# Kernel tuning notes

Hardware: AMD Instinct MI355X
Metric: run time of the kernel (lower is better)

Reference implementation:

```python
import jax, jax.numpy as jnp
import numpy as np

B, H_IMG, W_IMG, K = 4, 60, 80, 8
HW = H_IMG * W_IMG
IMG_D, PT_D = 192, 128
NH, DH = 6, 64
INNER = NH * DH
NHF = 6
POS_D = 2 * (2 * NHF + 1)  # harmonic emb of 2-d offset, append_input=True -> 26
MAX_DIST = 0.1


def setup_inputs() -> dict:
    key = jax.random.key(0)
    ks = jax.random.split(key, 6)
    ys, xs = jnp.meshgrid(jnp.linspace(0.0, 1.0, H_IMG), jnp.linspace(0.0, 1.0, W_IMG), indexing='ij')
    img_uv = jnp.stack([xs.reshape(-1), ys.reshape(-1)], axis=-1)  # [HW, 2], normalized pixel grid
    return {
        'feat_2d': jax.random.normal(ks[0], (B, HW, IMG_D), jnp.float32),
        'feat_3d': jax.random.normal(ks[1], (B, HW, PT_D), jnp.float32),
        'proj_uv': jax.random.uniform(ks[2], (B, HW, 2), dtype=jnp.float32),
        'img_uv': img_uv,
        'ln_gamma': jnp.ones((IMG_D,), jnp.float32),
        'q_gamma': jnp.ones((NH, DH), jnp.float32),
        'k_gamma': jnp.ones((NH, DH), jnp.float32),
        'Wq': jax.random.normal(ks[3], (IMG_D, INNER), jnp.float32) * IMG_D ** -0.5,
        'Wkv': jax.random.normal(ks[4], (PT_D + POS_D, 2 * INNER), jnp.float32) * (PT_D + POS_D) ** -0.5,
        'Wout': jax.random.normal(ks[5], (INNER, INNER), jnp.float32) * INNER ** -0.5,
    }


def _layernorm(x, g, eps=1e-5):
    mu = jnp.mean(x, -1, keepdims=True)
    var = jnp.mean((x - mu) ** 2, -1, keepdims=True)
    return (x - mu) * jax.lax.rsqrt(var + eps) * g


def _rmsnorm(x, g):
    # lucidrains-style query/key RMSNorm: l2-normalize last dim, scale by sqrt(dim) * per-head gamma
    n = jnp.maximum(jnp.linalg.norm(x, axis=-1, keepdims=True), 1e-12)
    return x / n * (DH ** 0.5) * g


def reference(feat_2d, feat_3d, proj_uv, img_uv, ln_gamma, q_gamma, k_gamma, Wq, Wkv, Wout):
    # --- kNN: for each image pixel, k nearest projected points (brute force) ---
    d2 = (jnp.sum(img_uv ** 2, -1)[None, :, None]
          + jnp.sum(proj_uv ** 2, -1)[:, None, :]
          - 2.0 * jnp.einsum('qd,bnd->bqn', img_uv, proj_uv))  # [B, HW, HW]
    idx = jax.lax.top_k(-d2, K)[1]  # [B, HW, K] int32 indices

    # --- gather neighbor uv coords and 3d features ---
    knn_uv = img_uv[idx]                                        # [B, HW, K, 2]
    knn_f3 = jnp.take_along_axis(feat_3d, idx.reshape(B, HW * K, 1), axis=1).reshape(B, HW, K, PT_D)
    offset = knn_uv - img_uv[None, :, None, :]                  # [B, HW, K, 2]
    mask = jnp.sum(offset ** 2, -1) <= MAX_DIST ** 2            # [B, HW, K]

    # --- harmonic positional embedding of offsets ---
    freqs = 2.0 ** jnp.arange(NHF, dtype=jnp.float32)
    e = (offset[..., None] * freqs).reshape(B, HW, K, 2 * NHF)
    pos = jnp.concatenate([jnp.sin(e), jnp.cos(e), offset], -1)  # [B, HW, K, 26]

    # --- Q / K / V projections ---
    q = (_layernorm(feat_2d, ln_gamma) @ Wq).reshape(B, HW, NH, DH)
    kv = jnp.concatenate([knn_f3, pos], -1) @ Wkv               # [B, HW, K, 2*INNER]
    k_, v_ = jnp.split(kv, 2, axis=-1)
    k_ = k_.reshape(B, HW, K, NH, DH)
    v_ = v_.reshape(B, HW, K, NH, DH)
    q = _rmsnorm(q, q_gamma)
    k_ = _rmsnorm(k_, k_gamma)

    # --- tiny per-pixel attention (query len 1, key len K), scale=1.0 ---
    scores = jnp.einsum('bnhd,bnkhd->bnhk', q, k_)              # [B, HW, NH, K]
    scores = jnp.where(mask[:, :, None, :], scores, -1e30)
    attn = jax.nn.softmax(scores, axis=-1)
    out = jnp.einsum('bnhk,bnkhd->bnhd', attn, v_).reshape(B, HW, INNER)
    return out @ Wout  # output_type='1d': [B, HW, INNER]
```

## Files before the change

### kernel.cpp

```cpp
#include <hip/hip_runtime.h>
#include <math.h>

#define B_    4
#define HW_   4800
#define K_    8
#define IMGD  192
#define PTD   128
#define NH_   6
#define DH_   64
#define INNER 384
#define KVIN  154
#define QT    8
#define NJ    64
#define XBS   168
#define AST   392
#define KTQ   6
#define KTK   5
#define KTO   12

#define GC    64
#define NCELL (GC * GC)
#define CS    (1.0f / 64.0f)

typedef _Float16 f16;
typedef __attribute__((ext_vector_type(8))) _Float16 f16x8;
typedef __attribute__((ext_vector_type(4))) float f32x4;

__global__ __launch_bounds__(256) void pack_kernel(
    const float* __restrict__ Wq, const float* __restrict__ Wkv,
    const float* __restrict__ Wout, f16* __restrict__ pw)
{
  const int e = blockIdx.x * 256 + threadIdx.x;
  if (e >= 672 * 512) return;
  const int f = e >> 9, r = e & 511, l = r >> 3, j = r & 7;
  const int lm = l & 15, kin = (l >> 4) * 8 + j;
  float v;
  if (f < 144) {
    const int nt = f / 6, kt = f % 6;
    v = Wq[(size_t)(kt * 32 + kin) * INNER + nt * 16 + lm];
  } else if (f < 264) {
    const int g = f - 144, nt = g / 5, kt = g % 5, k = kt * 32 + kin;
    v = (k < KVIN) ? Wkv[(size_t)k * (2 * INNER) + nt * 16 + lm] : 0.f;
  } else if (f < 384) {
    const int g = f - 264, nt = g / 5, kt = g % 5, k = kt * 32 + kin;
    v = (k < KVIN) ? Wkv[(size_t)k * (2 * INNER) + INNER + nt * 16 + lm] : 0.f;
  } else {
    const int g = f - 384, nt = g / 12, kt = g % 12;
    v = Wout[(size_t)(kt * 32 + kin) * INNER + nt * 16 + lm];
  }
  pw[e] = (f16)v;
}

__global__ __launch_bounds__(1024) void build_kernel(
    const float* __restrict__ proj_uv,
    float2* __restrict__ spts,
    unsigned short* __restrict__ sidx,
    unsigned short* __restrict__ cstart)
{
  __shared__ unsigned cnt[NCELL];
  __shared__ unsigned start[NCELL];
  __shared__ unsigned wsum[16];

  const int b   = blockIdx.x;
  const int tid = threadIdx.x;
  const int lane = tid & 63, wid = tid >> 6;
  const float2* pv = reinterpret_cast<const float2*>(proj_uv + (size_t)b * HW_ * 2);

  for (int c = tid; c < NCELL; c += 1024) cnt[c] = 0u;
  __syncthreads();

  for (int i = tid; i < HW_; i += 1024) {
    const float2 p = pv[i];
    const int cx = min(GC - 1, max(0, (int)(p.x * GC)));
    const int cy = min(GC - 1, max(0, (int)(p.y * GC)));
    atomicAdd(&cnt[cy * GC + cx], 1u);
  }
  __syncthreads();

  const int c0 = tid * 4;
  const unsigned v0 = cnt[c0], v1 = cnt[c0 + 1], v2 = cnt[c0 + 2], v3 = cnt[c0 + 3];
  const unsigned mysum = v0 + v1 + v2 + v3;
  unsigned inc = mysum;
#pragma unroll
  for (int off = 1; off < 64; off <<= 1) {
    const unsigned u = (unsigned)__shfl_up((int)inc, off);
    if (lane >= off) inc += u;
  }
  if (lane == 63) wsum[wid] = inc;
  __syncthreads();
  if (tid == 0) {
    unsigned s = 0;
#pragma unroll
    for (int wv = 0; wv < 16; ++wv) { const unsigned t = wsum[wv]; wsum[wv] = s; s += t; }
  }
  __syncthreads();
  unsigned base = wsum[wid] + inc - mysum;
  start[c0] = base;
  start[c0 + 1] = base + v0;
  start[c0 + 2] = base + v0 + v1;
  start[c0 + 3] = base + v0 + v1 + v2;
  unsigned short* cs = cstart + (size_t)b * (NCELL + 1);
  cs[c0]     = (unsigned short)start[c0];
  cs[c0 + 1] = (unsigned short)start[c0 + 1];
  cs[c0 + 2] = (unsigned short)start[c0 + 2];
  cs[c0 + 3] = (unsigned short)start[c0 + 3];
  if (tid == 0) cs[NCELL] = (unsigned short)HW_;
  __syncthreads();

  for (int i = tid; i < HW_; i += 1024) {
    const float2 p = pv[i];
    const int cx = min(GC - 1, max(0, (int)(p.x * GC)));
    const int cy = min(GC - 1, max(0, (int)(p.y * GC)));
    const unsigned slot = atomicAdd(&start[cy * GC + cx], 1u);
    spts[(size_t)b * HW_ + slot] = p;
    sidx[(size_t)b * HW_ + slot] = (unsigned short)i;
  }
}

#define SCAN_CELL(cyv, cxv)                                                   \
  {                                                                           \
    const int c = (cyv) * GC + (cxv);                                         \
    const int s0 = s_cs[c], s1 = s_cs[c + 1];                                 \
    for (int s = s0; s < s1; ++s) {                                           \
      const float2 p = s_p[s];                                                \
      const int n = (int)s_i[s];                                              \
      const float sqp = p.x * p.x + p.y * p.y;                \
      const float dot = fmaf(qy, p.y, qx * p.x);            \
      const float d   = (sqq + sqp) - 2.0f * dot;                             \
      const bool enter = (d < dist[K_ - 1]) ||                                \
                         (d == dist[K_ - 1] && n < ind[K_ - 1]);              \
      if (enter) {                                                            \
        bool placed = false;                                                  \
        _Pragma("unroll")                                                     \
        for (int t = K_ - 1; t >= 1; --t) {                                   \
          if (!placed) {                                                      \
            const bool lt = (d < dist[t - 1]) ||                              \
                            (d == dist[t - 1] && n < ind[t - 1]);             \
            if (lt) { dist[t] = dist[t - 1]; ind[t] = ind[t - 1]; }           \
            else    { dist[t] = d; ind[t] = n; placed = true; }               \
          }                                                                   \
        }                                                                     \
        if (!placed) { dist[0] = d; ind[0] = n; }                             \
      }                                                                       \
    }                                                                         \
  }

__global__ __launch_bounds__(256) void knn_kernel(
    const float* __restrict__ img_uv,
    const float2* __restrict__ spts,
    const unsigned short* __restrict__ sidx,
    const unsigned short* __restrict__ cstart,
    int* __restrict__ idx_out)
{
#pragma clang fp contract(off)
  __shared__ float2 s_p[HW_];
  __shared__ unsigned short s_i[HW_];
  __shared__ unsigned short s_cs[NCELL + 1];

  const int tid = threadIdx.x;
  const int b   = blockIdx.y;
  const int q   = blockIdx.x * 256 + tid;

  {
    const float2* gp = spts + (size_t)b * HW_;
    const unsigned short* gi = sidx + (size_t)b * HW_;
    const unsigned short* gc = cstart + (size_t)b * (NCELL + 1);
    for (int i = tid; i < HW_; i += 256) { s_p[i] = gp[i]; s_i[i] = gi[i]; }
    for (int i = tid; i < NCELL + 1; i += 256) s_cs[i] = gc[i];
  }
  __syncthreads();
  if (q >= HW_) return;

  const float qx = img_uv[q * 2 + 0];
  const float qy = img_uv[q * 2 + 1];
  const float sqq = qx * qx + qy * qy;

  const int cellx = min(GC - 1, max(0, (int)(qx * GC)));
  const int celly = min(GC - 1, max(0, (int)(qy * GC)));

  float dist[K_];
  int   ind[K_];
#pragma unroll
  for (int s = 0; s < K_; ++s) { dist[s] = 3.4e38f; ind[s] = 0x7fffffff; }

  for (int r = 0; r < GC; ++r) {
    if (r >= 2 && dist[K_ - 1] < 1e38f) {
      const float rb = (float)(r - 1) * CS;
      if (rb * rb > dist[K_ - 1] + 1e-4f) break;
    }
    const int ylo = max(0, celly - r), yhi = min(GC - 1, celly + r);
    for (int cy = ylo; cy <= yhi; ++cy) {
      const bool edge = (cy == celly - r) || (cy == celly + r);
      if (edge) {
        const int xlo = max(0, cellx - r), xhi = min(GC - 1, cellx + r);
        for (int cx = xlo; cx <= xhi; ++cx) SCAN_CELL(cy, cx);
      } else {
        if (cellx - r >= 0)      SCAN_CELL(cy, cellx - r);
        if (cellx + r <= GC - 1) SCAN_CELL(cy, cellx + r);
      }
    }
  }

  int* dst = idx_out + ((size_t)b * HW_ + q) * K_;
#pragma unroll
  for (int s = 0; s < K_; ++s) dst[s] = ind[s];
}

__global__ __launch_bounds__(256, 3) void fused_kernel(
    const float* __restrict__ feat_2d,
    const float* __restrict__ feat_3d,
    const float* __restrict__ img_uv,
    const float* __restrict__ ln_gamma,
    const float* __restrict__ q_gamma,
    const float* __restrict__ k_gamma,
    const f16*   __restrict__ pw,
    const int*   __restrict__ idx_ws,
    float* __restrict__ out)
{
  __shared__ alignas(16) f16   s_X[NJ][XBS];
  __shared__ alignas(16) float s_regA[QT * AST];
  __shared__ alignas(16) float s_attn[QT][NH_][K_];
  __shared__ alignas(16) float s_kss[NJ][NH_];
  __shared__ alignas(16) float s_ksc[NJ][NH_];
  __shared__ float s_qss[QT][NH_];
  __shared__ float s_mask[NJ];
  __shared__ int   s_idx[NJ];
  __shared__ float s_offx[NJ];
  __shared__ float s_offy[NJ];

  f16* s_f16 = reinterpret_cast<f16*>(s_regA);

  const int tid = threadIdx.x;
  const int b   = blockIdx.y;
  const int bx  = (blockIdx.x & 7) * 75 + (blockIdx.x >> 3);
  const int q0  = bx * QT;
  const int l   = tid & 63;
  const int w   = tid >> 6;
  const int lm  = l & 15;
  const int lg  = l >> 4;

  const f16* pwq = pw;
  const f16* pwk = pw + 144 * 512;
  const f16* pwv = pw + 264 * 512;
  const f16* pwo = pw + 384 * 512;

  if (tid < NJ) {
    const int j  = tid;
    const int q  = q0 + (j >> 3);
    const int id = idx_ws[((size_t)b * HW_ + q) * K_ + (j & 7)];
    s_idx[j] = id;
    const float ax = img_uv[id * 2], ay = img_uv[id * 2 + 1];
    const float bx2 = img_uv[q * 2], by2 = img_uv[q * 2 + 1];
    s_offx[j] = ax - bx2; s_offy[j] = ay - by2;
    const double dox = (double)ax - (double)bx2;
    const double doy = (double)ay - (double)by2;
    s_mask[j] = (dox * dox + doy * doy <= 0.010000000000000002) ? 1.f : 0.f;
  }
  {
    unsigned* z = (unsigned*)(s_f16 + 8 * AST);
    for (int o = tid; o < 4 * AST; o += 256) z[o] = 0u;
  }
  if (tid < QT * NH_) s_qss[tid / NH_][tid % NH_] = 0.f;
  for (int o = tid; o < NJ * NH_; o += 256) {
    s_kss[o / NH_][o % NH_] = 0.f;
    s_ksc[o / NH_][o % NH_] = 0.f;
  }
  {
    const int r  = ((tid >> 6) << 1) | ((tid >> 5) & 1);
    const int sl = tid & 31;
    const float* row = feat_2d + ((size_t)b * HW_ + q0 + r) * IMGD;
    float x[6]; float sum = 0.f, ssq = 0.f;
#pragma unroll
    for (int i = 0; i < 6; ++i) { x[i] = row[sl + 32 * i]; sum += x[i]; ssq += x[i] * x[i]; }
#pragma unroll
    for (int m = 16; m >= 1; m >>= 1) { sum += __shfl_xor(sum, m); ssq += __shfl_xor(ssq, m); }
    const float mu = sum * (1.f / 192.f);
    float var = ssq * (1.f / 192.f) - mu * mu;
    var = fmaxf(var, 0.f);
    const float rstd = rsqrtf(var + 1e-5f);
#pragma unroll
    for (int i = 0; i < 6; ++i) {
      const int c = sl + 32 * i;
      s_f16[r * AST + c] = (f16)((x[i] - mu) * rstd * ln_gamma[c]);
    }
  }
  __syncthreads();

  const int jX = tid >> 2, tsub = tid & 3;
  float4 xf[8];
  {
    const float4* f4 = reinterpret_cast<const float4*>(
        feat_3d + ((size_t)b * HW_ + s_idx[jX]) * PTD) + tsub * 8;
#pragma unroll
    for (int i = 0; i < 8; ++i) xf[i] = f4[i];
  }
  f32x4 qacc[6];
#pragma unroll
  for (int t = 0; t < 6; ++t) qacc[t] = (f32x4){0.f, 0.f, 0.f, 0.f};
  {
    const f16* ar = s_f16 + lm * AST + lg * 8;
    f16x8 acur = *(const f16x8*)(ar);
    f16x8 bcur[6], bnxt[6];
#pragma unroll
    for (int t = 0; t < 6; ++t)
      bcur[t] = *(const f16x8*)(pwq + ((((w * 6 + t) * 6 + 0) << 6) + l) * 8);
#pragma unroll
    for (int kt = 0; kt < KTQ; ++kt) {
      f16x8 anxt;
      if (kt < KTQ - 1) {
        anxt = *(const f16x8*)(ar + (kt + 1) * 32);
#pragma unroll
        for (int t = 0; t < 6; ++t)
          bnxt[t] = *(const f16x8*)(pwq + ((((w * 6 + t) * 6 + kt + 1) << 6) + l) * 8);
      }
#pragma unroll
      for (int t = 0; t < 6; ++t)
        qacc[t] = __builtin_amdgcn_mfma_f32_16x16x32_f16(acur, bcur[t], qacc[t], 0, 0, 0);
      if (kt < KTQ - 1) {
        acur = anxt;
#pragma unroll
        for (int t = 0; t < 6; ++t) bcur[t] = bnxt[t];
      }
    }
  }
  {
    f16* xr = &s_X[jX][tsub * 32];
#pragma unroll
    for (int i = 0; i < 8; ++i) {
      xr[i * 4 + 0] = (f16)xf[i].x; xr[i * 4 + 1] = (f16)xf[i].y;
      xr[i * 4 + 2] = (f16)xf[i].z; xr[i * 4 + 3] = (f16)xf[i].w;
    }
    if (tsub == 0) {
      const float ox = s_offx[jX], oy = s_offy[jX];
      f16* xp = &s_X[jX][PTD];
#pragma unroll
      for (int m = 0; m < 6; ++m) {
        const float fr = (float)(1 << m);
        float sx, cx, sy, cy;
        sincosf(ox * fr, &sx, &cx);
        sincosf(oy * fr, &sy, &cy);
        xp[m] = (f16)sx; xp[6 + m] = (f16)sy;
        xp[12 + m] = (f16)cx; xp[18 + m] = (f16)cy;
      }
      xp[24] = (f16)ox; xp[25] = (f16)oy;
#pragma unroll
      for (int m = 26; m < 32; ++m) xp[m] = (f16)0.f;
    }
  }
  __syncthreads();

  if (lg < 2) {
    const int h0w = (w * 6) >> 2;
    float s2a[4], s2b[4];
#pragma unroll
    for (int reg = 0; reg < 4; ++reg) { s2a[reg] = 0.f; s2b[reg] = 0.f; }
#pragma unroll
    for (int t = 0; t < 6; ++t) {
      const int hi = ((w * 6 + t) >> 2) - h0w;
#pragma unroll
      for (int reg = 0; reg < 4; ++reg) {
        const float v = qacc[t][reg];
        s_regA[(lg * 4 + reg) * AST + (w * 6 + t) * 16 + lm] = v;
        if (hi == 0) s2a[reg] += v * v; else s2b[reg] += v * v;
      }
    }
#pragma unroll
    for (int reg = 0; reg < 4; ++reg) {
      atomicAdd(&s_qss[lg * 4 + reg][h0w], s2a[reg]);
      atomicAdd(&s_qss[lg * 4 + reg][h0w + 1], s2b[reg]);
    }
  }
  __syncthreads();

  {
    f16x8 af[4][KTK];
#pragma unroll
    for (int mt = 0; mt < 4; ++mt) {
      const f16* xh = &s_X[16 * mt + lm][lg * 8];
#pragma unroll
      for (int kt = 0; kt < KTK; ++kt) af[mt][kt] = *(const f16x8*)(xh + kt * 32);
    }
    f16x8 bcur[KTK], bnxt[KTK];
#pragma unroll
    for (int kt = 0; kt < KTK; ++kt)
      bcur[kt] = *(const f16x8*)(pwk + (((w * KTK + kt) << 6) + l) * 8);
#pragma unroll
    for (int h = 0; h < NH_; ++h) {
      if (h < NH_ - 1) {
        const int ntn = (h + 1) * 4 + w;
#pragma unroll
        for (int kt = 0; kt < KTK; ++kt)
          bnxt[kt] = *(const f16x8*)(pwk + (((ntn * KTK + kt) << 6) + l) * 8);
      }
      const int nt  = h * 4 + w;
      const int col = nt * 16 + lm;
      const float gg = k_gamma[col] * q_gamma[col];
      f32x4 c[4];
#pragma unroll
      for (int mt = 0; mt < 4; ++mt) c[mt] = (f32x4){0.f, 0.f, 0.f, 0.f};
#pragma unroll
      for (int kt = 0; kt < KTK; ++kt)
#pragma unroll
        for (int mt = 0; mt < 4; ++mt)
          c[mt] = __builtin_amdgcn_mfma_f32_16x16x32_f16(af[mt][kt], bcur[kt], c[mt], 0, 0, 0);
#pragma unroll
      for (int mt = 0; mt < 4; ++mt) {
        const int rq = 2 * mt + (lg >> 1);
        const float nnq = fmaxf(sqrtf(s_qss[rq][h]), 1e-12f);
        const float qg = s_regA[rq * AST + col] * (8.f / nnq) * gg;
        float ss[4], sc[4];
#pragma unroll
        for (int reg = 0; reg < 4; ++reg) {
          const float v = c[mt][reg];
          ss[reg] = v * v; sc[reg] = v * qg;
        }
#pragma unroll
        for (int m = 1; m < 16; m <<= 1) {
#pragma unroll
          for (int reg = 0; reg < 4; ++reg) {
            ss[reg] += __shfl_xor(ss[reg], m);
            sc[reg] += __shfl_xor(sc[reg], m);
          }
        }
        if (lm == 0) {
#pragma unroll
          for (int reg = 0; reg < 4; ++reg) {
            const int row = 16 * mt + 4 * lg + reg;
            atomicAdd(&s_kss[row][h], ss[reg]);
            atomicAdd(&s_ksc[row][h], sc[reg]);
          }
        }
      }
      if (h < NH_ - 1) {
#pragma unroll
        for (int kt = 0; kt < KTK; ++kt) bcur[kt] = bnxt[kt];
      }
    }
  }
  __syncthreads();

  if (tid < QT * NH_) {
    const int r = tid / NH_, h = tid % NH_;
    float s[K_]; float mx = -1e38f;
#pragma unroll
    for (int k = 0; k < K_; ++k) {
      const int row = r * K_ + k;
      const float nn = fmaxf(sqrtf(s_kss[row][h]), 1e-12f);
      float v = (8.f / nn) * s_ksc[row][h];
      if (s_mask[row] == 0.f) v = -1e30f;
      s[k] = v; mx = fmaxf(mx, v);
    }
    float sum = 0.f;
#pragma unroll
    for (int k = 0; k < K_; ++k) { const float pp = expf(s[k] - mx); s[k] = pp; sum += pp; }
    const float inv = 1.f / sum;
#pragma unroll
    for (int k = 0; k < K_; ++k) s_attn[r][h][k] = s[k] * inv;
  }
  __syncthreads();

  {
    unsigned* z = (unsigned*)(s_f16 + 8 * AST);
    for (int o = tid; o < 4 * AST; o += 256) z[o] = 0u;
  }
  f16x8 xbv[4];
#pragma unroll
  for (int rep = 0; rep < 4; ++rep) {
    const int task = tid + 256 * rep;
    if (task < 960) {
      const int p = task / 320, rem = task - p * 320;
      const int r16 = rem / 20, cb = rem - r16 * 20;
      const int q = r16 & 7, hh = 2 * p + (r16 >> 3);
      const float4 a0 = *(const float4*)&s_attn[q][hh][0];
      const float4 a1 = *(const float4*)&s_attn[q][hh][4];
      const float av[8] = {a0.x, a0.y, a0.z, a0.w, a1.x, a1.y, a1.z, a1.w};
      float acc[8];
#pragma unroll
      for (int e = 0; e < 8; ++e) acc[e] = 0.f;
#pragma unroll
      for (int k = 0; k < 8; ++k) {
        const f16x8 xv = *(const f16x8*)&s_X[q * 8 + k][cb * 8];
#pragma unroll
        for (int e = 0; e < 8; ++e) acc[e] += av[k] * (float)xv[e];
      }
      f16x8 rr;
#pragma unroll
      for (int e = 0; e < 8; ++e) rr[e] = (f16)acc[e];
      xbv[rep] = rr;
    }
  }
  __syncthreads();
#pragma unroll
  for (int rep = 0; rep < 4; ++rep) {
    const int task = tid + 256 * rep;
    if (task < 960) {
      const int p = task / 320, rem = task - p * 320;
      const int r16 = rem / 20, cb = rem - r16 * 20;
      *(f16x8*)&s_X[p * 16 + r16][cb * 8] = xbv[rep];
    }
  }
  __syncthreads();

  {
#pragma unroll
    for (int p = 0; p < 3; ++p) {
      f16x8 af[KTK];
#pragma unroll
      for (int kt = 0; kt < KTK; ++kt)
        af[kt] = *(const f16x8*)&s_X[p * 16 + lm][lg * 8 + kt * 32];
#pragma unroll
      for (int ii = 0; ii < 2; ++ii) {
        const int nt = w + 4 * (2 * p + ii);
        const int h  = nt >> 2;
        f32x4 c = (f32x4){0.f, 0.f, 0.f, 0.f};
#pragma unroll
        for (int kt = 0; kt < KTK; ++kt) {
          const f16x8 bf = *(const f16x8*)(pwv + (((nt * KTK + kt) << 6) + l) * 8);
          c = __builtin_amdgcn_mfma_f32_16x16x32_f16(af[kt], bf, c, 0, 0, 0);
        }
        if ((lg >> 1) == (h & 1)) {
#pragma unroll
          for (int reg = 0; reg < 4; ++reg) {
            const int q = (lg * 4 + reg) & 7;
            s_f16[q * AST + nt * 16 + lm] = (f16)c[reg];
          }
        }
      }
    }
  }
  __syncthreads();

  {
    f32x4 oacc[6];
#pragma unroll
    for (int t = 0; t < 6; ++t) oacc[t] = (f32x4){0.f, 0.f, 0.f, 0.f};
    const f16* ar = s_f16 + lm * AST + lg * 8;
    f16x8 acur = *(const f16x8*)(ar);
    f16x8 bcur[6], bnxt[6];
#pragma unroll
    for (int t = 0; t < 6; ++t)
      bcur[t] = *(const f16x8*)(pwo + ((((w * 6 + t) * 12 + 0) << 6) + l) * 8);
#pragma unroll
    for (int kt = 0; kt < KTO; ++kt) {
      f16x8 anxt;
      if (kt < KTO - 1) {
        anxt = *(const f16x8*)(ar + (kt + 1) * 32);
#pragma unroll
        for (int t = 0; t < 6; ++t)
          bnxt[t] = *(const f16x8*)(pwo + ((((w * 6 + t) * 12 + kt + 1) << 6) + l) * 8);
      }
#pragma unroll
      for (int t = 0; t < 6; ++t)
        oacc[t] = __builtin_amdgcn_mfma_f32_16x16x32_f16(acur, bcur[t], oacc[t], 0, 0, 0);
      if (kt < KTO - 1) {
        acur = anxt;
#pragma unroll
        for (int t = 0; t < 6; ++t) bcur[t] = bnxt[t];
      }
    }
    if (lg < 2) {
      float* orow0 = out + ((size_t)b * HW_ + q0) * INNER;
#pragma unroll
      for (int reg = 0; reg < 4; ++reg) {
        const int m = lg * 4 + reg;
#pragma unroll
        for (int t = 0; t < 6; ++t) {
          orow0[(size_t)m * INNER + (w * 6 + t) * 16 + lm] = oacc[t][reg];
        }
      }
    }
  }
}

extern "C" void kernel_launch(void* const* d_in, const int* in_sizes, int n_in,
                              void* d_out, int out_size, void* d_ws, size_t ws_size,
                              hipStream_t stream) {
  (void)in_sizes; (void)n_in; (void)out_size; (void)ws_size;
  const float* feat_2d = (const float*)d_in[0];
  const float* feat_3d = (const float*)d_in[1];
  const float* proj_uv = (const float*)d_in[2];
  const float* img_uv  = (const float*)d_in[3];
  const float* ln_g    = (const float*)d_in[4];
  const float* q_g     = (const float*)d_in[5];
  const float* k_g     = (const float*)d_in[6];
  const float* Wq      = (const float*)d_in[7];
  const float* Wkv     = (const float*)d_in[8];
  const float* Wout    = (const float*)d_in[9];
  float* out = (float*)d_out;

  int* idx_ws = (int*)d_ws;
  f16* pw = (f16*)((char*)d_ws + 614400);
  float2* spts = (float2*)((char*)d_ws + 1302528);
  unsigned short* sidx = (unsigned short*)((char*)d_ws + 1456128);
  unsigned short* cstart = (unsigned short*)((char*)d_ws + 1494528);

  pack_kernel<<<dim3(1344), 256, 0, stream>>>(Wq, Wkv, Wout, pw);
  build_kernel<<<dim3(B_), 1024, 0, stream>>>(proj_uv, spts, sidx, cstart);
  knn_kernel<<<dim3((HW_ + 255) / 256, B_), 256, 0, stream>>>(
      img_uv, spts, sidx, cstart, idx_ws);
  fused_kernel<<<dim3(HW_ / QT, B_), 256, 0, stream>>>(
      feat_2d, feat_3d, img_uv, ln_g, q_g, k_g, pw, idx_ws, out);
}
```

Baseline: 261.9 us.

## Double query tile to 16 pixels per block to fill MFMA rows

Raises the per-block query tile from 8 to 16 pixels (128 neighbor rows), so the 16-row MFMA tiles for Q, output and V projections are fully used instead of half-padded with zeros. The zero-fill of padding rows goes away, K-projection weights are held in registers across 8 row tiles, and the V step is restructured per head. The trade is roughly doubled shared memory and register use per block, so occupancy drops from 3 to 2 blocks per CU, and the block-to-XCD remap is reworked for 300 blocks.

After: 292.3 us. +11.6%, slower.

```diff
diff --git a/kernel.cpp b/kernel.cpp
--- a/kernel.cpp
+++ b/kernel.cpp
@@ -10,8 +10,8 @@
 #define DH_   64
 #define INNER 384
 #define KVIN  154
-#define QT    8
-#define NJ    64
+#define QT    16
+#define NJ    128
 #define XBS   168
 #define AST   392
 #define KTQ   6
@@ -206,7 +206,7 @@
   for (int s = 0; s < K_; ++s) dst[s] = ind[s];
 }
 
-__global__ __launch_bounds__(256, 3) void fused_kernel(
+__global__ __launch_bounds__(256, 2) void fused_kernel(
     const float* __restrict__ feat_2d,
     const float* __restrict__ feat_3d,
     const float* __restrict__ img_uv,
@@ -232,7 +232,9 @@
 
   const int tid = threadIdx.x;
   const int b   = blockIdx.y;
-  const int bx  = (blockIdx.x & 7) * 75 + (blockIdx.x >> 3);
+  const int orig = blockIdx.x;
+  const int xcd  = orig & 7, id8 = orig >> 3;
+  const int bx   = (xcd < 4) ? xcd * 38 + id8 : 152 + (xcd - 4) * 37 + id8;
   const int q0  = bx * QT;
   const int l   = tid & 63;
   const int w   = tid >> 6;
@@ -256,79 +258,48 @@
     const double doy = (double)ay - (double)by2;
     s_mask[j] = (dox * dox + doy * doy <= 0.010000000000000002) ? 1.f : 0.f;
   }
-  {
-    unsigned* z = (unsigned*)(s_f16 + 8 * AST);
-    for (int o = tid; o < 4 * AST; o += 256) z[o] = 0u;
-  }
   if (tid < QT * NH_) s_qss[tid / NH_][tid % NH_] = 0.f;
   for (int o = tid; o < NJ * NH_; o += 256) {
     s_kss[o / NH_][o % NH_] = 0.f;
     s_ksc[o / NH_][o % NH_] = 0.f;
   }
   {
-    const int r  = ((tid >> 6) << 1) | ((tid >> 5) & 1);
-    const int sl = tid & 31;
+    const int r  = tid >> 4;
+    const int sl = tid & 15;
     const float* row = feat_2d + ((size_t)b * HW_ + q0 + r) * IMGD;
-    float x[6]; float sum = 0.f, ssq = 0.f;
-#pragma unroll
-    for (int i = 0; i < 6; ++i) { x[i] = row[sl + 32 * i]; sum += x[i]; ssq += x[i] * x[i]; }
-#pragma unroll
-    for (int m = 16; m >= 1; m >>= 1) { sum += __shfl_xor(sum, m); ssq += __shfl_xor(ssq, m); }
+    float x[12]; float sum = 0.f, ssq = 0.f;
+#pragma unroll
+    for (int i = 0; i < 12; ++i) { x[i] = row[sl + 16 * i]; sum += x[i]; ssq += x[i] * x[i]; }
+#pragma unroll
+    for (int m = 8; m >= 1; m >>= 1) { sum += __shfl_xor(sum, m); ssq += __shfl_xor(ssq, m); }
     const float mu = sum * (1.f / 192.f);
     float var = ssq * (1.f / 192.f) - mu * mu;
     var = fmaxf(var, 0.f);
     const float rstd = rsqrtf(var + 1e-5f);
 #pragma unroll
-    for (int i = 0; i < 6; ++i) {
-      const int c = sl + 32 * i;
+    for (int i = 0; i < 12; ++i) {
+      const int c = sl + 16 * i;
       s_f16[r * AST + c] = (f16)((x[i] - mu) * rstd * ln_gamma[c]);
     }
   }
   __syncthreads();
 
-  const int jX = tid >> 2, tsub = tid & 3;
-  float4 xf[8];
+  const int jX = tid >> 1, tsub = tid & 1;
   {
     const float4* f4 = reinterpret_cast<const float4*>(
-        feat_3d + ((size_t)b * HW_ + s_idx[jX]) * PTD) + tsub * 8;
-#pragma unroll
-    for (int i = 0; i < 8; ++i) xf[i] = f4[i];
-  }
-  f32x4 qacc[6];
-#pragma unroll
-  for (int t = 0; t < 6; ++t) qacc[t] = (f32x4){0.f, 0.f, 0.f, 0.f};
-  {
-    const f16* ar = s_f16 + lm * AST + lg * 8;
-    f16x8 acur = *(const f16x8*)(ar);
-    f16x8 bcur[6], bnxt[6];
-#pragma unroll
-    for (int t = 0; t < 6; ++t)
-      bcur[t] = *(const f16x8*)(pwq + ((((w * 6 + t) * 6 + 0) << 6) + l) * 8);
-#pragma unroll
-    for (int kt = 0; kt < KTQ; ++kt) {
-      f16x8 anxt;
-      if (kt < KTQ - 1) {
-        anxt = *(const f16x8*)(ar + (kt + 1) * 32);
-#pragma unroll
-        for (int t = 0; t < 6; ++t)
-          bnxt[t] = *(const f16x8*)(pwq + ((((w * 6 + t) * 6 + kt + 1) << 6) + l) * 8);
-      }
-#pragma unroll
-      for (int t = 0; t < 6; ++t)
-        qacc[t] = __builtin_amdgcn_mfma_f32_16x16x32_f16(acur, bcur[t], qacc[t], 0, 0, 0);
-      if (kt < KTQ - 1) {
-        acur = anxt;
-#pragma unroll
-        for (int t = 0; t < 6; ++t) bcur[t] = bnxt[t];
-      }
-    }
-  }
-  {
-    f16* xr = &s_X[jX][tsub * 32];
-#pragma unroll
-    for (int i = 0; i < 8; ++i) {
-      xr[i * 4 + 0] = (f16)xf[i].x; xr[i * 4 + 1] = (f16)xf[i].y;
-      xr[i * 4 + 2] = (f16)xf[i].z; xr[i * 4 + 3] = (f16)xf[i].w;
+        feat_3d + ((size_t)b * HW_ + s_idx[jX]) * PTD) + tsub * 16;
+    f16* xr = &s_X[jX][tsub * 64];
+#pragma unroll
+    for (int half = 0; half < 2; ++half) {
+      float4 xf[8];
+#pragma unroll
+      for (int i = 0; i < 8; ++i) xf[i] = f4[half * 8 + i];
+#pragma unroll
+      for (int i = 0; i < 8; ++i) {
+        const int c = half * 32 + i * 4;
+        xr[c + 0] = (f16)xf[i].x; xr[c + 1] = (f16)xf[i].y;
+        xr[c + 2] = (f16)xf[i].z; xr[c + 3] = (f16)xf[i].w;
+      }
     }
     if (tsub == 0) {
       const float ox = s_offx[jX], oy = s_offy[jX];
@@ -347,9 +318,38 @@
       for (int m = 26; m < 32; ++m) xp[m] = (f16)0.f;
     }
   }
-  __syncthreads();
-
-  if (lg < 2) {
+  f32x4 qacc[6];
+#pragma unroll
+  for (int t = 0; t < 6; ++t) qacc[t] = (f32x4){0.f, 0.f, 0.f, 0.f};
+  {
+    const f16* ar = s_f16 + lm * AST + lg * 8;
+    f16x8 acur = *(const f16x8*)(ar);
+    f16x8 bcur[6], bnxt[6];
+#pragma unroll
+    for (int t = 0; t < 6; ++t)
+      bcur[t] = *(const f16x8*)(pwq + ((((w * 6 + t) * 6 + 0) << 6) + l) * 8);
+#pragma unroll
+    for (int kt = 0; kt < KTQ; ++kt) {
+      f16x8 anxt;
+      if (kt < KTQ - 1) {
+        anxt = *(const f16x8*)(ar + (kt + 1) * 32);
+#pragma unroll
+        for (int t = 0; t < 6; ++t)
+          bnxt[t] = *(const f16x8*)(pwq + ((((w * 6 + t) * 6 + kt + 1) << 6) + l) * 8);
+      }
+#pragma unroll
+      for (int t = 0; t < 6; ++t)
+        qacc[t] = __builtin_amdgcn_mfma_f32_16x16x32_f16(acur, bcur[t], qacc[t], 0, 0, 0);
+      if (kt < KTQ - 1) {
+        acur = anxt;
+#pragma unroll
+        for (int t = 0; t < 6; ++t) bcur[t] = bnxt[t];
+      }
+    }
+  }
+  __syncthreads();
+
+  {
     const int h0w = (w * 6) >> 2;
     float s2a[4], s2b[4];
 #pragma unroll
@@ -373,45 +373,36 @@
   __syncthreads();
 
   {
-    f16x8 af[4][KTK];
-#pragma unroll
-    for (int mt = 0; mt < 4; ++mt) {
+    f16x8 bk[NH_][KTK];
+#pragma unroll
+    for (int h = 0; h < NH_; ++h) {
+      const int nt = h * 4 + w;
+#pragma unroll
+      for (int kt = 0; kt < KTK; ++kt)
+        bk[h][kt] = *(const f16x8*)(pwk + (((nt * KTK + kt) << 6) + l) * 8);
+    }
+#pragma unroll
+    for (int mt = 0; mt < 8; ++mt) {
       const f16* xh = &s_X[16 * mt + lm][lg * 8];
-#pragma unroll
-      for (int kt = 0; kt < KTK; ++kt) af[mt][kt] = *(const f16x8*)(xh + kt * 32);
-    }
-    f16x8 bcur[KTK], bnxt[KTK];
-#pragma unroll
-    for (int kt = 0; kt < KTK; ++kt)
-      bcur[kt] = *(const f16x8*)(pwk + (((w * KTK + kt) << 6) + l) * 8);
-#pragma unroll
-    for (int h = 0; h < NH_; ++h) {
-      if (h < NH_ - 1) {
-        const int ntn = (h + 1) * 4 + w;
+      f16x8 af[KTK];
+#pragma unroll
+      for (int kt = 0; kt < KTK; ++kt) af[kt] = *(const f16x8*)(xh + kt * 32);
+      const int rq = 2 * mt + (lg >> 1);
+#pragma unroll
+      for (int h = 0; h < NH_; ++h) {
+        const int nt  = h * 4 + w;
+        const int col = nt * 16 + lm;
+        f32x4 c = (f32x4){0.f, 0.f, 0.f, 0.f};
 #pragma unroll
         for (int kt = 0; kt < KTK; ++kt)
-          bnxt[kt] = *(const f16x8*)(pwk + (((ntn * KTK + kt) << 6) + l) * 8);
-      }
-      const int nt  = h * 4 + w;
-      const int col = nt * 16 + lm;
-      const float gg = k_gamma[col] * q_gamma[col];
-      f32x4 c[4];
-#pragma unroll
-      for (int mt = 0; mt < 4; ++mt) c[mt] = (f32x4){0.f, 0.f, 0.f, 0.f};
-#pragma unroll
-      for (int kt = 0; kt < KTK; ++kt)
-#pragma unroll
-        for (int mt = 0; mt < 4; ++mt)
-          c[mt] = __builtin_amdgcn_mfma_f32_16x16x32_f16(af[mt][kt], bcur[kt], c[mt], 0, 0, 0);
-#pragma unroll
-      for (int mt = 0; mt < 4; ++mt) {
-        const int rq = 2 * mt + (lg >> 1);
+          c = __builtin_amdgcn_mfma_f32_16x16x32_f16(af[kt], bk[h][kt], c, 0, 0, 0);
         const float nnq = fmaxf(sqrtf(s_qss[rq][h]), 1e-12f);
-        const float qg = s_regA[rq * AST + col] * (8.f / nnq) * gg;
+        const float qg = s_regA[rq * AST + col] * (8.f / nnq)
+                         * k_gamma[col] * q_gamma[col];
         float ss[4], sc[4];
 #pragma unroll
         for (int reg = 0; reg < 4; ++reg) {
-          const float v = c[mt][reg];
+          const float v = c[reg];
           ss[reg] = v * v; sc[reg] = v * qg;
         }
 #pragma unroll
@@ -431,10 +422,6 @@
           }
         }
       }
-      if (h < NH_ - 1) {
-#pragma unroll
-        for (int kt = 0; kt < KTK; ++kt) bcur[kt] = bnxt[kt];
-      }
     }
   }
   __syncthreads();
@@ -459,20 +446,15 @@
   }
   __syncthreads();
 
-  {
-    unsigned* z = (unsigned*)(s_f16 + 8 * AST);
-    for (int o = tid; o < 4 * AST; o += 256) z[o] = 0u;
-  }
-  f16x8 xbv[4];
-#pragma unroll
-  for (int rep = 0; rep < 4; ++rep) {
+  f16x8 xbv[8];
+#pragma unroll
+  for (int rep = 0; rep < 8; ++rep) {
     const int task = tid + 256 * rep;
-    if (task < 960) {
-      const int p = task / 320, rem = task - p * 320;
-      const int r16 = rem / 20, cb = rem - r16 * 20;
-      const int q = r16 & 7, hh = 2 * p + (r16 >> 3);
-      const float4 a0 = *(const float4*)&s_attn[q][hh][0];
-      const float4 a1 = *(const float4*)&s_attn[q][hh][4];
+    if (task < 1920) {
+      const int rhq = task / 20, cb = task - rhq * 20;
+      const int h = rhq >> 4, q = rhq & 15;
+      const float4 a0 = *(const float4*)&s_attn[q][h][0];
+      const float4 a1 = *(const float4*)&s_attn[q][h][4];
       const float av[8] = {a0.x, a0.y, a0.z, a0.w, a1.x, a1.y, a1.z, a1.w};
       float acc[8];
 #pragma unroll
@@ -491,40 +473,33 @@
   }
   __syncthreads();
 #pragma unroll
-  for (int rep = 0; rep < 4; ++rep) {
+  for (int rep = 0; rep < 8; ++rep) {
     const int task = tid + 256 * rep;
-    if (task < 960) {
-      const int p = task / 320, rem = task - p * 320;
-      const int r16 = rem / 20, cb = rem - r16 * 20;
-      *(f16x8*)&s_X[p * 16 + r16][cb * 8] = xbv[rep];
-    }
-  }
-  __syncthreads();
-
-  {
-#pragma unroll
-    for (int p = 0; p < 3; ++p) {
+    if (task < 1920) {
+      const int rhq = task / 20, cb = task - rhq * 20;
+      *(f16x8*)&s_X[rhq][cb * 8] = xbv[rep];
+    }
+  }
+  __syncthreads();
+
+  {
+#pragma unroll
+    for (int h = 0; h < NH_; ++h) {
+      const int nt = h * 4 + w;
+      const f16* xh = &s_X[h * 16 + lm][lg * 8];
       f16x8 af[KTK];
 #pragma unroll
-      for (int kt = 0; kt < KTK; ++kt)
-        af[kt] = *(const f16x8*)&s_X[p * 16 + lm][lg * 8 + kt * 32];
-#pragma unroll
-      for (int ii = 0; ii < 2; ++ii) {
-        const int nt = w + 4 * (2 * p + ii);
-        const int h  = nt >> 2;
-        f32x4 c = (f32x4){0.f, 0.f, 0.f, 0.f};
-#pragma unroll
-        for (int kt = 0; kt < KTK; ++kt) {
-          const f16x8 bf = *(const f16x8*)(pwv + (((nt * KTK + kt) << 6) + l) * 8);
-          c = __builtin_amdgcn_mfma_f32_16x16x32_f16(af[kt], bf, c, 0, 0, 0);
-        }
-        if ((lg >> 1) == (h & 1)) {
-#pragma unroll
-          for (int reg = 0; reg < 4; ++reg) {
-            const int q = (lg * 4 + reg) & 7;
-            s_f16[q * AST + nt * 16 + lm] = (f16)c[reg];
-          }
-        }
+      for (int kt = 0; kt < KTK; ++kt) af[kt] = *(const f16x8*)(xh + kt * 32);
+      f32x4 c = (f32x4){0.f, 0.f, 0.f, 0.f};
+#pragma unroll
+      for (int kt = 0; kt < KTK; ++kt) {
+        const f16x8 bf = *(const f16x8*)(pwv + (((nt * KTK + kt) << 6) + l) * 8);
+        c = __builtin_amdgcn_mfma_f32_16x16x32_f16(af[kt], bf, c, 0, 0, 0);
+      }
+#pragma unroll
+      for (int reg = 0; reg < 4; ++reg) {
+        const int q = lg * 4 + reg;
+        s_f16[q * AST + nt * 16 + lm] = (f16)c[reg];
       }
     }
   }
@@ -558,7 +533,7 @@
         for (int t = 0; t < 6; ++t) bcur[t] = bnxt[t];
       }
     }
-    if (lg < 2) {
+    {
       float* orow0 = out + ((size_t)b * HW_ + q0) * INNER;
 #pragma unroll
       for (int reg = 0; reg < 4; ++reg) {
```
